# Performance work log

Measured on AMD Instinct MI355X. Metric: run time of the kernel, lower is better.

Reference implementation:

```python
import jax, jax.numpy as jnp
import numpy as np

DIM = 1024
HEADS = 8
HEAD_DIM = DIM // HEADS
FFN = 4096
B, N = 32, 1024
EPS = 1e-5


def layer_norm(x, g, b):
    mu = jnp.mean(x, axis=-1, keepdims=True)
    var = jnp.mean(jnp.square(x - mu), axis=-1, keepdims=True)
    return (x - mu) * jax.lax.rsqrt(var + EPS) * g + b


def setup_inputs() -> dict:
    key = jax.random.key(0)
    ks = jax.random.split(key, 10)
    s = 0.02
    return {
        "x": jax.random.normal(ks[0], (B, N, DIM), dtype=jnp.float32),
        "haltingscore": jnp.zeros((B, N), dtype=jnp.float32),
        "Wq": jax.random.normal(ks[1], (DIM, DIM), dtype=jnp.float32) * s,
        "Wkv": jax.random.normal(ks[2], (DIM, 2 * DIM), dtype=jnp.float32) * s,
        "Wp": jax.random.normal(ks[3], (DIM, DIM), dtype=jnp.float32) * s,
        "bp": jnp.zeros((DIM,), dtype=jnp.float32),
        "W1": jax.random.normal(ks[4], (DIM, FFN), dtype=jnp.float32) * s,
        "b1": jnp.zeros((FFN,), dtype=jnp.float32),
        "W2": jax.random.normal(ks[5], (FFN, DIM), dtype=jnp.float32) * s,
        "b2": jnp.zeros((DIM,), dtype=jnp.float32),
        "ln1_g": jnp.ones((DIM,), dtype=jnp.float32),
        "ln1_b": jnp.zeros((DIM,), dtype=jnp.float32),
        "ln2_g": jnp.ones((DIM,), dtype=jnp.float32),
        "ln2_b": jnp.zeros((DIM,), dtype=jnp.float32),
    }


def reference(x, haltingscore, Wq, Wkv, Wp, bp, W1, b1, W2, b2,
              ln1_g, ln1_b, ln2_g, ln2_b):
    b, n, c = x.shape
    scale = HEAD_DIM ** -0.5
    # ---- EfficientAttention (explicit QK^T softmax V) ----
    q = (x @ Wq).reshape(b, n, HEADS, HEAD_DIM).transpose(0, 2, 1, 3)  # bhnd
    kv = (x @ Wkv).reshape(b, n, 2, HEADS, HEAD_DIM).transpose(2, 0, 3, 1, 4)
    k, v = kv[0], kv[1]                                               # bhnd
    attn = jax.nn.softmax(jnp.einsum('bhnd,bhmd->bhnm', q, k) * scale, axis=-1)
    o = jnp.einsum('bhnm,bhmd->bhnd', attn, v)
    o = o.transpose(0, 2, 1, 3).reshape(b, n, c)
    o = o @ Wp + bp
    attn_mean = jnp.mean(attn, axis=1)                                # (B, N, N)
    # ---- residual + LN1 ----
    h = layer_norm(x + o, ln1_g, ln1_b)
    # ---- FFN + residual + LN2 ----
    ff = jax.nn.relu(h @ W1 + b1) @ W2 + b2
    out = layer_norm(h + ff, ln2_g, ln2_b)
    # ---- halting score update ----
    a = jax.nn.softmax(jnp.sum(attn_mean, axis=1), axis=-1)           # (B, N)
    halting = haltingscore + a
    return (out, halting, a)
```

## Files before the change

### kernel.cpp

```cpp
#include <hip/hip_runtime.h>
#include <hip/hip_bf16.h>
#include <stdint.h>

#define DIMC 1024
#define HEADS 8
#define HDIM 128
#define FFND 4096
#define BATCH 32
#define SEQ 1024
#define SROWS (BATCH*SEQ)
#define QSTR 3072

typedef unsigned short u16;
typedef short short4v __attribute__((ext_vector_type(4)));
typedef short short8 __attribute__((ext_vector_type(8)));
typedef float f32x4 __attribute__((ext_vector_type(4)));
typedef __bf16 bf16x8 __attribute__((ext_vector_type(8)));
typedef unsigned uintv2 __attribute__((ext_vector_type(2)));

__device__ __forceinline__ u16 f2bf(float f) {
    union { float f; uint32_t u; } x{f};
    uint32_t r = x.u + 0x7FFFu + ((x.u >> 16) & 1u);
    return (u16)(r >> 16);
}
__device__ __forceinline__ float bf2f(u16 h) {
    union { uint32_t u; float f; } x;
    x.u = ((uint32_t)h) << 16;
    return x.f;
}

__device__ __forceinline__ f32x4 mfma16(short8 a, short8 b, f32x4 c) {
    return __builtin_amdgcn_mfma_f32_16x16x32_bf16(
        __builtin_bit_cast(bf16x8, a), __builtin_bit_cast(bf16x8, b), c, 0, 0, 0);
}

__device__ __forceinline__ void gload_lds16(const u16* g, u16* lds) {
    __builtin_amdgcn_global_load_lds(
        (const __attribute__((address_space(1))) uint32_t*)g,
        (__attribute__((address_space(3))) uint32_t*)lds, 16, 0, 0);
}

#define DPP_RORADD(x, ctrl) do {                                               \
    int _t = __builtin_amdgcn_mov_dpp(__builtin_bit_cast(int, (x)), (ctrl),    \
                                      0xf, 0xf, true);                         \
    (x) += __builtin_bit_cast(float, _t); } while (0)

__device__ __forceinline__ short8 p2frag(f32x4 p0, f32x4 p1, int lane) {
    uint32_t a, b, c, d;
    asm("v_cvt_pk_bf16_f32 %0, %1, %2" : "=v"(a) : "v"(p0[0]), "v"(p0[1]));
    asm("v_cvt_pk_bf16_f32 %0, %1, %2" : "=v"(b) : "v"(p0[2]), "v"(p0[3]));
    asm("v_cvt_pk_bf16_f32 %0, %1, %2" : "=v"(c) : "v"(p1[0]), "v"(p1[1]));
    asm("v_cvt_pk_bf16_f32 %0, %1, %2" : "=v"(d) : "v"(p1[2]), "v"(p1[3]));
    uint32_t P, Q, R, S;
#if __has_builtin(__builtin_amdgcn_permlane32_swap)
    {
        uintv2 pq = __builtin_amdgcn_permlane32_swap(a, c, false, false);
        uintv2 rs = __builtin_amdgcn_permlane32_swap(b, d, false, false);
        P = pq[0]; Q = pq[1]; R = rs[0]; S = rs[1];
    }
#else
    {
        uint32_t ax = (uint32_t)__shfl_xor((int)a, 32);
        uint32_t bx = (uint32_t)__shfl_xor((int)b, 32);
        uint32_t cx = (uint32_t)__shfl_xor((int)c, 32);
        uint32_t dx = (uint32_t)__shfl_xor((int)d, 32);
        const bool up = (lane & 32) != 0;
        P = up ? cx : a; Q = up ? c : ax;
        R = up ? dx : b; S = up ? d : bx;
    }
#endif
    uint32_t w0, w1, w2, w3;
#if __has_builtin(__builtin_amdgcn_permlane16_swap)
    {
        uintv2 w02 = __builtin_amdgcn_permlane16_swap(P, Q, false, false);
        uintv2 w13 = __builtin_amdgcn_permlane16_swap(R, S, false, false);
        w0 = w02[0]; w2 = w02[1]; w1 = w13[0]; w3 = w13[1];
    }
#else
    {
        uint32_t Px = (uint32_t)__shfl_xor((int)P, 16);
        uint32_t Qx = (uint32_t)__shfl_xor((int)Q, 16);
        uint32_t Rx = (uint32_t)__shfl_xor((int)R, 16);
        uint32_t Sx = (uint32_t)__shfl_xor((int)S, 16);
        const bool odd = (lane & 16) != 0;
        w0 = odd ? Qx : P;  w1 = odd ? Sx : R;
        w2 = odd ? Q  : Px; w3 = odd ? S  : Rx;
    }
#endif
    union { uint32_t w[4]; short8 s; } u;
    u.w[0] = w0; u.w[1] = w1; u.w[2] = w2; u.w[3] = w3;
    return u.s;
}

__global__ __launch_bounds__(256) void k_cast(const float* __restrict__ in,
                                              u16* __restrict__ out, int n4) {
    int i = blockIdx.x * 256 + threadIdx.x;
    if (i < n4) {
        f32x4 v = ((const f32x4*)in)[i];
        uint32_t lo = f2bf(v[0]) | ((uint32_t)f2bf(v[1]) << 16);
        uint32_t hi = f2bf(v[2]) | ((uint32_t)f2bf(v[3]) << 16);
        ((uint2*)out)[i] = make_uint2(lo, hi);
    }
}

__global__ __launch_bounds__(256) void k_transpose_cast(const float* __restrict__ W,
                                                        u16* __restrict__ Wt,
                                                        int K, int N) {
    __shared__ u16 tile[32][33];
    int n0 = blockIdx.x * 32, k0 = blockIdx.y * 32;
    int tx = threadIdx.x, ty = threadIdx.y;
#pragma unroll
    for (int i = 0; i < 32; i += 8)
        tile[ty + i][tx] = f2bf(W[(size_t)(k0 + ty + i) * N + n0 + tx]);
    __syncthreads();
#pragma unroll
    for (int i = 0; i < 32; i += 8)
        Wt[(size_t)(n0 + ty + i) * K + k0 + tx] = tile[tx][ty + i];
}

template<bool OUT_BF16, bool RELU, bool BIAS, bool VSPLIT>
__global__ __launch_bounds__(512, 2) void k_gemm256(const u16* __restrict__ A,
                                                    const u16* __restrict__ Bt,
                                                    const float* __restrict__ bias,
                                                    void* __restrict__ C,
                                                    u16* __restrict__ Vt,
                                                    int M, int N, int K, int lda) {
    union Smem {
        struct { u16 A[4][8192]; u16 B[4][8192]; } k;
        u16 ob[64 * 264];
        float of[64 * 268];
        u16 vt[256 * 66];
    };
    __shared__ Smem smem;
    const int tid = threadIdx.x;
    const int lane = tid & 63, wv = tid >> 6;
    const int wm = wv >> 2, wn = wv & 3;
    const int l15 = lane & 15, lg = lane >> 4;
    const int gx = gridDim.x;
    const int nwg = gx * gridDim.y;
    const int id = blockIdx.y * gx + blockIdx.x;
    const int id2 = (id & 7) * (nwg >> 3) + (id >> 3);
    const int row0 = (id2 / gx) << 8, col0 = (id2 % gx) << 8;
    const int NT = K >> 5;

#define STAGE_A(tt) {                                                          \
    int _t = (tt);                                                             \
    _Pragma("unroll")                                                          \
    for (int i = 0; i < 2; ++i) {                                              \
        int blk = wv * 2 + i;                                                  \
        gload_lds16(A + (size_t)(row0 + blk * 16 + l15) * lda + _t * 32 + lg * 8,\
                    &smem.k.A[_t & 3][blk * 512]);                             \
    } }
#define STAGE_B(tt) {                                                          \
    int _t = (tt);                                                             \
    _Pragma("unroll")                                                          \
    for (int i = 0; i < 2; ++i) {                                              \
        int blk = wv * 2 + i;                                                  \
        gload_lds16(Bt + (size_t)(col0 + blk * 16 + l15) * K + _t * 32 + lg * 8,\
                    &smem.k.B[_t & 3][blk * 512]);                             \
    } }

    STAGE_A(0); STAGE_B(0);
    STAGE_A(1); STAGE_B(1);
    STAGE_A(2); STAGE_B(2);

    f32x4 acc[8][4] = {};
    for (int t = 0; t < NT; ++t) {
        const int slot = t & 3;
        if (t <= NT - 3)      asm volatile("s_waitcnt vmcnt(8)" ::: "memory");
        else if (t == NT - 2) asm volatile("s_waitcnt vmcnt(4)" ::: "memory");
        else                  asm volatile("s_waitcnt vmcnt(0)" ::: "memory");
        __builtin_amdgcn_s_barrier();
        __builtin_amdgcn_sched_barrier(0);

        const u16* Ab = &smem.k.A[slot][(wm * 8) * 512];
        const u16* Bb = &smem.k.B[slot][(wn * 4) * 512];

        if (t + 3 < NT) STAGE_A(t + 3);
        short8 bf[4], af[4];
#pragma unroll
        for (int n = 0; n < 4; ++n) bf[n] = *(const short8*)(Bb + n * 512 + lane * 8);
#pragma unroll
        for (int m = 0; m < 4; ++m) af[m] = *(const short8*)(Ab + m * 512 + lane * 8);
        __builtin_amdgcn_s_setprio(1);
#pragma unroll
        for (int m = 0; m < 4; ++m)
#pragma unroll
            for (int n = 0; n < 4; ++n)
                acc[m][n] = mfma16(af[m], bf[n], acc[m][n]);
        __builtin_amdgcn_s_setprio(0);

        if (t + 3 < NT) STAGE_B(t + 3);
#pragma unroll
        for (int m = 0; m < 4; ++m) af[m] = *(const short8*)(Ab + (4 + m) * 512 + lane * 8);
        __builtin_amdgcn_s_setprio(1);
#pragma unroll
        for (int m = 0; m < 4; ++m)
#pragma unroll
            for (int n = 0; n < 4; ++n)
                acc[4 + m][n] = mfma16(af[m], bf[n], acc[4 + m][n]);
        __builtin_amdgcn_s_setprio(0);
    }
#undef STAGE_A
#undef STAGE_B

    const bool vpath = VSPLIT && (col0 >= 2048);
    __syncthreads();
#pragma unroll
    for (int s = 0; s < 4; ++s) {
        if (s) __syncthreads();
        if (wm == (s >> 1)) {
            const int mb4 = (s & 1) * 4;
#pragma unroll
            for (int mm = 0; mm < 4; ++mm)
#pragma unroll
                for (int n = 0; n < 4; ++n) {
                    int c = wn * 64 + n * 16 + l15;
                    float bv = BIAS ? bias[col0 + c] : 0.f;
#pragma unroll
                    for (int j = 0; j < 4; ++j) {
                        int lr = mm * 16 + lg * 4 + j;
                        float v = acc[mb4 + mm][n][j] + bv;
                        if (RELU) v = fmaxf(v, 0.f);
                        if (vpath)         smem.vt[c * 66 + lr] = f2bf(v);
                        else if (OUT_BF16) smem.ob[lr * 264 + c] = f2bf(v);
                        else               smem.of[lr * 268 + c] = v;
                    }
                }
        }
        __syncthreads();
        const int gr0 = row0 + s * 64;
        if (vpath) {
            const int bb = gr0 >> 10;
            const int mb = gr0 & 1023;
#pragma unroll
            for (int it = 0; it < 4; ++it) {
                int idx = it * 512 + tid;
                int dc = idx >> 3, mseg = idx & 7;
                int hh = (col0 - 2048 + dc) >> 7;
                int dd = (col0 - 2048 + dc) & 127;
                *(short8*)(Vt + ((size_t)(bb * 8 + hh)) * (HDIM * SEQ)
                              + (size_t)dd * SEQ + mb + mseg * 8) =
                    *(const short8*)(&smem.vt[dc * 66 + mseg * 8]);
            }
        } else if (OUT_BF16) {
#pragma unroll
            for (int it = 0; it < 4; ++it) {
                int idx = it * 512 + tid;
                int r = idx >> 5, seg = idx & 31;
                *(short8*)((u16*)C + (size_t)(gr0 + r) * N + col0 + seg * 8) =
                    *(const short8*)(&smem.ob[r * 264 + seg * 8]);
            }
        } else {
#pragma unroll
            for (int it = 0; it < 8; ++it) {
                int idx = it * 512 + tid;
                int r = idx >> 6, seg = idx & 63;
                *(f32x4*)((float*)C + (size_t)(gr0 + r) * N + col0 + seg * 4) =
                    *(const f32x4*)(&smem.of[r * 268 + seg * 4]);
            }
        }
    }
}

__global__ __launch_bounds__(256, 3) void k_attn(const u16* __restrict__ QKV,
                                                 const u16* __restrict__ Vt,
                                                 u16* __restrict__ O,
                                                 float* __restrict__ csp) {
    union Sm {
        u16 K2[2][8192];
        struct { u16 Kl[2][4096]; u16 Vl[2][4096]; } pb;
    };
    __shared__ Sm sm;
    __shared__ float cs[1024];
    const int id = blockIdx.x;
    const int id2 = (id & 7) * 256 + (id >> 3);
    const int qt = id2 & 7, bh = id2 >> 3;
    const int b = bh >> 3, h = bh & 7;
    const int tid = threadIdx.x, lane = tid & 63, wv = tid >> 6;
    const int l15 = lane & 15, lg = lane >> 4;

    for (int i = tid; i < 1024; i += 256) cs[i] = 0.f;

    const int q0 = qt * 128 + wv * 32;
    const u16* qbaseA = QKV + (size_t)(b * SEQ + q0 + l15) * QSTR + h * HDIM + lg * 8;
    const u16* qbaseB = qbaseA + (size_t)16 * QSTR;
    short8 qfA[4], qfB[4];
#pragma unroll
    for (int kk = 0; kk < 4; ++kk) {
        qfA[kk] = *(const short8*)(qbaseA + kk * 32);
        qfB[kk] = *(const short8*)(qbaseB + kk * 32);
    }
    const float CEXP = 0.12751743f;
    const u16* kbase = QKV + (size_t)(b * SEQ) * QSTR + 1024 + h * HDIM;
    const u16* vtb = Vt + (size_t)bh * HDIM * SEQ;

#define STAGE_K2(tt) { _Pragma("unroll")                                        \
    for (int i = 0; i < 4; ++i) {                                               \
        gload_lds16(kbase + (size_t)((tt) * 64 + wv * 16 + l15) * QSTR          \
                    + i * 32 + lg * 8, &sm.K2[(tt) & 1][(wv * 4 + i) * 512]); } }
#define STAGE_K(tt) { _Pragma("unroll")                                         \
    for (int i = 0; i < 2; ++i) { int c = wv * 2 + i;                           \
        gload_lds16(kbase + (size_t)((tt) * 32 + (c >> 2) * 16 + l15) * QSTR    \
                    + (c & 3) * 32 + lg * 8, &sm.pb.Kl[(tt) & 1][c * 512]); } }
#define STAGE_V(tt) { _Pragma("unroll")                                         \
    for (int i = 0; i < 2; ++i) { int c = wv * 2 + i;                           \
        gload_lds16(vtb + (size_t)(c * 16 + l15) * SEQ + (tt) * 32 + lg * 8,    \
                    &sm.pb.Vl[(tt) & 1][c * 512]); } }

    STAGE_K2(0);
    asm volatile("s_waitcnt vmcnt(0)" ::: "memory");
    __builtin_amdgcn_s_barrier();
    f32x4 rsA4 = {0.f, 0.f, 0.f, 0.f}, rsB4 = {0.f, 0.f, 0.f, 0.f};
    for (int t = 0; t < 16; ++t) {
        if (t < 15) STAGE_K2(t + 1);
        const u16* Kp = &sm.K2[t & 1][0];
        __builtin_amdgcn_s_setprio(1);
#pragma unroll
        for (int j = 0; j < 4; j += 2) {
            f32x4 s0 = {0.f,0.f,0.f,0.f}, s1 = {0.f,0.f,0.f,0.f};
            f32x4 s2 = {0.f,0.f,0.f,0.f}, s3 = {0.f,0.f,0.f,0.f};
#pragma unroll
            for (int kk = 0; kk < 4; ++kk) {
                short8 k0 = *(const short8*)(Kp + (j * 4 + kk) * 512 + lane * 8);
                short8 k1 = *(const short8*)(Kp + ((j + 1) * 4 + kk) * 512 + lane * 8);
                s0 = mfma16(k0, qfA[kk], s0);
                s1 = mfma16(k0, qfB[kk], s1);
                s2 = mfma16(k1, qfA[kk], s2);
                s3 = mfma16(k1, qfB[kk], s3);
            }
#pragma unroll
            for (int r = 0; r < 4; ++r) {
                rsA4[r] += __builtin_amdgcn_exp2f(s0[r] * CEXP)
                         + __builtin_amdgcn_exp2f(s2[r] * CEXP);
                rsB4[r] += __builtin_amdgcn_exp2f(s1[r] * CEXP)
                         + __builtin_amdgcn_exp2f(s3[r] * CEXP);
            }
        }
        __builtin_amdgcn_s_setprio(0);
        asm volatile("s_waitcnt vmcnt(0)" ::: "memory");
        __builtin_amdgcn_s_barrier();
    }
    float rsA = (rsA4[0] + rsA4[1]) + (rsA4[2] + rsA4[3]);
    float rsB = (rsB4[0] + rsB4[1]) + (rsB4[2] + rsB4[3]);
    rsA += __shfl_xor(rsA, 16); rsA += __shfl_xor(rsA, 32);
    rsB += __shfl_xor(rsB, 16); rsB += __shfl_xor(rsB, 32);
    const float lgA = __builtin_amdgcn_logf(rsA);
    const float lgB = __builtin_amdgcn_logf(rsB);

    STAGE_K(0); STAGE_V(0);
    asm volatile("s_waitcnt vmcnt(0)" ::: "memory");
    __builtin_amdgcn_s_barrier();
    f32x4 odA[8] = {}, odB[8] = {};
    for (int t = 0; t < 32; ++t) {
        const int m0 = t * 32;
        if (t < 31) { STAGE_K(t + 1); STAGE_V(t + 1); }
        const u16* Kp = &sm.pb.Kl[t & 1][0];
        f32x4 sA0 = {0.f,0.f,0.f,0.f}, sA1 = {0.f,0.f,0.f,0.f};
        f32x4 sB0 = {0.f,0.f,0.f,0.f}, sB1 = {0.f,0.f,0.f,0.f};
        __builtin_amdgcn_s_setprio(1);
#pragma unroll
        for (int kk = 0; kk < 4; ++kk) {
            short8 k0 = *(const short8*)(Kp + kk * 512 + lane * 8);
            short8 k1 = *(const short8*)(Kp + (4 + kk) * 512 + lane * 8);
            sA0 = mfma16(k0, qfA[kk], sA0);
            sA1 = mfma16(k1, qfA[kk], sA1);
            sB0 = mfma16(k0, qfB[kk], sB0);
            sB1 = mfma16(k1, qfB[kk], sB1);
        }
        __builtin_amdgcn_s_setprio(0);
        f32x4 pA0, pA1, pB0, pB1;
#pragma unroll
        for (int r = 0; r < 4; ++r) {
            pA0[r] = __builtin_amdgcn_exp2f(__builtin_fmaf(sA0[r], CEXP, -lgA));
            pA1[r] = __builtin_amdgcn_exp2f(__builtin_fmaf(sA1[r], CEXP, -lgA));
            pB0[r] = __builtin_amdgcn_exp2f(__builtin_fmaf(sB0[r], CEXP, -lgB));
            pB1[r] = __builtin_amdgcn_exp2f(__builtin_fmaf(sB1[r], CEXP, -lgB));
        }
        float csv[8];
#pragma unroll
        for (int r = 0; r < 4; ++r) {
            csv[r]     = pA0[r] + pB0[r];
            csv[4 + r] = pA1[r] + pB1[r];
        }
#pragma unroll
        for (int j2 = 0; j2 < 8; ++j2) {
            DPP_RORADD(csv[j2], 0x128);
            DPP_RORADD(csv[j2], 0x124);
            DPP_RORADD(csv[j2], 0x122);
            DPP_RORADD(csv[j2], 0x121);
        }
        float cval = csv[0];
        cval = (l15 == 1) ? csv[1] : cval;
        cval = (l15 == 2) ? csv[2] : cval;
        cval = (l15 == 3) ? csv[3] : cval;
        cval = (l15 == 4) ? csv[4] : cval;
        cval = (l15 == 5) ? csv[5] : cval;
        cval = (l15 == 6) ? csv[6] : cval;
        cval = (l15 == 7) ? csv[7] : cval;
        if (l15 < 8) {
            int mw = (l15 < 4) ? (lg * 4 + l15) : (16 + lg * 4 + (l15 - 4));
            atomicAdd(&cs[m0 + mw], cval);
        }
        short8 paA = p2frag(pA0, pA1, lane);
        short8 paB = p2frag(pB0, pB1, lane);
        const u16* Vb_ = &sm.pb.Vl[t & 1][0];
        __builtin_amdgcn_s_setprio(1);
#pragma unroll
        for (int db = 0; db < 8; ++db) {
            short8 vf = *(const short8*)(Vb_ + db * 512 + lane * 8);
            odA[db] = mfma16(paA, vf, odA[db]);
            odB[db] = mfma16(paB, vf, odB[db]);
        }
        __builtin_amdgcn_s_setprio(0);
        asm volatile("s_waitcnt vmcnt(0)" ::: "memory");
        __builtin_amdgcn_s_barrier();
    }
#undef STAGE_K2
#undef STAGE_K
#undef STAGE_V
    __syncthreads();
    u16* obA = O + (size_t)(b * SEQ + q0 + lg * 4) * QSTR + h * HDIM + l15;
    u16* obB = obA + (size_t)16 * QSTR;
#pragma unroll
    for (int db = 0; db < 8; ++db)
#pragma unroll
        for (int r = 0; r < 4; ++r) {
            obA[(size_t)r * QSTR + db * 16] = f2bf(odA[db][r]);
            obB[(size_t)r * QSTR + db * 16] = f2bf(odB[db][r]);
        }
    for (int m = tid; m < 1024; m += 256)
        csp[((size_t)bh * 8 + qt) * 1024 + m] = cs[m];
}

__global__ __launch_bounds__(256) void k_ln1(u16* xio,
                                             const u16* __restrict__ pj,
                                             const float* __restrict__ g,
                                             const float* __restrict__ bt) {
    const int row = blockIdx.x;
    const int t = threadIdx.x, lane = t & 63, wv = t >> 6;
    short4v va = ((const short4v*)(xio + (size_t)row * DIMC))[t];
    short4v hv = ((const short4v*)(pj + (size_t)row * DIMC))[t];
    f32x4 s;
#pragma unroll
    for (int j = 0; j < 4; ++j) s[j] = bf2f((u16)va[j]) + bf2f((u16)hv[j]);
    float sum = s[0] + s[1] + s[2] + s[3];
    float sq = s[0]*s[0] + s[1]*s[1] + s[2]*s[2] + s[3]*s[3];
#pragma unroll
    for (int o = 1; o < 64; o <<= 1) { sum += __shfl_xor(sum, o); sq += __shfl_xor(sq, o); }
    __shared__ float red[8];
    if (lane == 0) { red[wv] = sum; red[4 + wv] = sq; }
    __syncthreads();
    sum = red[0] + red[1] + red[2] + red[3];
    sq  = red[4] + red[5] + red[6] + red[7];
    float mu = sum * (1.f / DIMC);
    float rstd = rsqrtf(sq * (1.f / DIMC) - mu * mu + 1e-5f);
    f32x4 gg = ((const f32x4*)g)[t];
    f32x4 bb = ((const f32x4*)bt)[t];
    uint32_t lo, hi;
    float o0 = (s[0] - mu) * rstd * gg[0] + bb[0];
    float o1 = (s[1] - mu) * rstd * gg[1] + bb[1];
    float o2 = (s[2] - mu) * rstd * gg[2] + bb[2];
    float o3 = (s[3] - mu) * rstd * gg[3] + bb[3];
    lo = f2bf(o0) | ((uint32_t)f2bf(o1) << 16);
    hi = f2bf(o2) | ((uint32_t)f2bf(o3) << 16);
    ((uint2*)(xio + (size_t)row * DIMC))[t] = make_uint2(lo, hi);
}

__global__ __launch_bounds__(256) void k_ln2(const u16* __restrict__ xa,
                                             const u16* __restrict__ f2,
                                             const float* __restrict__ g,
                                             const float* __restrict__ bt,
                                             float* __restrict__ of) {
    const int row = blockIdx.x;
    const int t = threadIdx.x, lane = t & 63, wv = t >> 6;
    short4v hv = ((const short4v*)(xa + (size_t)row * DIMC))[t];
    short4v fv = ((const short4v*)(f2 + (size_t)row * DIMC))[t];
    f32x4 s;
#pragma unroll
    for (int j = 0; j < 4; ++j) s[j] = bf2f((u16)hv[j]) + bf2f((u16)fv[j]);
    float sum = s[0] + s[1] + s[2] + s[3];
    float sq = s[0]*s[0] + s[1]*s[1] + s[2]*s[2] + s[3]*s[3];
#pragma unroll
    for (int o = 1; o < 64; o <<= 1) { sum += __shfl_xor(sum, o); sq += __shfl_xor(sq, o); }
    __shared__ float red[8];
    if (lane == 0) { red[wv] = sum; red[4 + wv] = sq; }
    __syncthreads();
    sum = red[0] + red[1] + red[2] + red[3];
    sq  = red[4] + red[5] + red[6] + red[7];
    float mu = sum * (1.f / DIMC);
    float rstd = rsqrtf(sq * (1.f / DIMC) - mu * mu + 1e-5f);
    f32x4 gg = ((const f32x4*)g)[t];
    f32x4 bb = ((const f32x4*)bt)[t];
    f32x4 o4;
#pragma unroll
    for (int j = 0; j < 4; ++j) o4[j] = (s[j] - mu) * rstd * gg[j] + bb[j];
    ((f32x4*)(of + (size_t)row * DIMC))[t] = o4;
}

__global__ __launch_bounds__(256) void k_halt(const float* __restrict__ csp,
                                              const float* __restrict__ hs,
                                              float* __restrict__ halt_out,
                                              float* __restrict__ a_out) {
    const int b = blockIdx.x, t = threadIdx.x, lane = t & 63, wv = t >> 6;
    const float* base = csp + (size_t)b * 65536;
    float acc[4] = {0.f, 0.f, 0.f, 0.f};
    for (int s2 = 0; s2 < 64; ++s2) {
#pragma unroll
        for (int j = 0; j < 4; ++j) acc[j] += base[(size_t)s2 * 1024 + j * 256 + t];
    }
    float mx = -1e30f;
#pragma unroll
    for (int j = 0; j < 4; ++j) { acc[j] *= 0.125f; mx = fmaxf(mx, acc[j]); }
#pragma unroll
    for (int o = 1; o < 64; o <<= 1) mx = fmaxf(mx, __shfl_xor(mx, o));
    __shared__ float red[8];
    if (lane == 0) red[wv] = mx;
    __syncthreads();
    mx = fmaxf(fmaxf(red[0], red[1]), fmaxf(red[2], red[3]));
    float e[4]; float sum = 0.f;
#pragma unroll
    for (int j = 0; j < 4; ++j) { e[j] = __expf(acc[j] - mx); sum += e[j]; }
#pragma unroll
    for (int o = 1; o < 64; o <<= 1) sum += __shfl_xor(sum, o);
    if (lane == 0) red[4 + wv] = sum;
    __syncthreads();
    sum = red[4] + red[5] + red[6] + red[7];
    float inv = 1.f / sum;
#pragma unroll
    for (int j = 0; j < 4; ++j) {
        int m = j * 256 + t;
        float a = e[j] * inv;
        a_out[b * SEQ + m] = a;
        halt_out[b * SEQ + m] = hs[b * SEQ + m] + a;
    }
}

extern "C" void kernel_launch(void* const* d_in, const int* in_sizes, int n_in,
                              void* d_out, int out_size, void* d_ws, size_t ws_size,
                              hipStream_t stream) {
    (void)in_sizes; (void)n_in; (void)out_size; (void)ws_size;
    const float* x   = (const float*)d_in[0];
    const float* hs  = (const float*)d_in[1];
    const float* Wq  = (const float*)d_in[2];
    const float* Wkv = (const float*)d_in[3];
    const float* Wp  = (const float*)d_in[4];
    const float* bp  = (const float*)d_in[5];
    const float* W1  = (const float*)d_in[6];
    const float* b1  = (const float*)d_in[7];
    const float* W2  = (const float*)d_in[8];
    const float* b2  = (const float*)d_in[9];
    const float* g1  = (const float*)d_in[10];
    const float* be1 = (const float*)d_in[11];
    const float* g2  = (const float*)d_in[12];
    const float* be2 = (const float*)d_in[13];

    float* out = (float*)d_out;
    float* halt_out = out + (size_t)SROWS * DIMC;
    float* a_out = halt_out + SROWS;

    char* w = (char*)d_ws;
    const size_t MB = 1024 * 1024;
    u16*  xb    = (u16*)(w);
    u16*  qkv   = (u16*)(w + 64 * MB);
    u16*  Vt    = (u16*)(w + 256 * MB);
    u16*  WqkvT = (u16*)(w + 320 * MB);
    u16*  WpT   = (u16*)(w + 326 * MB);
    u16*  W1T   = (u16*)(w + 328 * MB);
    u16*  W2T   = (u16*)(w + 336 * MB);
    float* csp  = (float*)(w + 344 * MB);
    u16*  o_b   = qkv + 2048;
    u16*  projb = (u16*)(w + 256 * MB);
    u16*  hb    = xb;
    u16*  ff1   = (u16*)(w + 64 * MB);
    u16*  ff2b  = (u16*)(w + 192 * MB);

    dim3 tb(32, 8);
    k_cast<<<SROWS * DIMC / 4 / 256, 256, 0, stream>>>(x, xb, SROWS * DIMC / 4);
    k_transpose_cast<<<dim3(DIMC / 32, DIMC / 32), tb, 0, stream>>>(Wq, WqkvT, DIMC, DIMC);
    k_transpose_cast<<<dim3(2 * DIMC / 32, DIMC / 32), tb, 0, stream>>>(
        Wkv, WqkvT + (size_t)DIMC * DIMC, DIMC, 2 * DIMC);
    k_transpose_cast<<<dim3(DIMC / 32, DIMC / 32), tb, 0, stream>>>(Wp, WpT, DIMC, DIMC);
    k_transpose_cast<<<dim3(FFND / 32, DIMC / 32), tb, 0, stream>>>(W1, W1T, DIMC, FFND);
    k_transpose_cast<<<dim3(DIMC / 32, FFND / 32), tb, 0, stream>>>(W2, W2T, FFND, DIMC);
    k_gemm256<true, false, false, true><<<dim3(QSTR / 256, SROWS / 256), 512, 0, stream>>>(
        xb, WqkvT, nullptr, qkv, Vt, SROWS, QSTR, DIMC, DIMC);
    k_attn<<<2048, 256, 0, stream>>>(qkv, Vt, o_b, csp);
    k_gemm256<true, false, true, false><<<dim3(DIMC / 256, SROWS / 256), 512, 0, stream>>>(
        o_b, WpT, bp, projb, nullptr, SROWS, DIMC, DIMC, QSTR);
    k_ln1<<<SROWS, 256, 0, stream>>>(xb, projb, g1, be1);
    for (int c = 0; c < 2; ++c) {
        const size_t ro = (size_t)c * 16384;
        k_gemm256<true, true, true, false><<<dim3(FFND / 256, 16384 / 256), 512, 0, stream>>>(
            hb + ro * DIMC, W1T, b1, ff1, nullptr, 16384, FFND, DIMC, DIMC);
        k_gemm256<true, false, true, false><<<dim3(DIMC / 256, 16384 / 256), 512, 0, stream>>>(
            ff1, W2T, b2, ff2b, nullptr, 16384, DIMC, FFND, FFND);
        k_ln2<<<16384, 256, 0, stream>>>(hb + ro * DIMC, ff2b, g2, be2, out + ro * DIMC);
    }
    k_halt<<<BATCH, 256, 0, stream>>>(csp, hs, halt_out, a_out);
}
```

Measured before the change: 1.433 ms.

## Add two-slot ring GEMM variant, merge FFN chunks, fuse W2 output into LN2

```diff
diff --git a/kernel.cpp b/kernel.cpp
--- a/kernel.cpp
+++ b/kernel.cpp
@@ -118,15 +118,16 @@
         Wt[(size_t)(n0 + ty + i) * K + k0 + tx] = tile[tx][ty + i];
 }
 
-template<bool OUT_BF16, bool RELU, bool BIAS, bool VSPLIT>
-__global__ __launch_bounds__(512, 2) void k_gemm256(const u16* __restrict__ A,
+template<bool OUT_BF16, bool RELU, bool BIAS, bool VSPLIT, int RING>
+__global__ __launch_bounds__(512, RING == 2 ? 4 : 2) void k_gemm256(
+                                                    const u16* __restrict__ A,
                                                     const u16* __restrict__ Bt,
                                                     const float* __restrict__ bias,
                                                     void* __restrict__ C,
                                                     u16* __restrict__ Vt,
                                                     int M, int N, int K, int lda) {
     union Smem {
-        struct { u16 A[4][8192]; u16 B[4][8192]; } k;
+        struct { u16 A[RING][8192]; u16 B[RING][8192]; } k;
         u16 ob[64 * 264];
         float of[64 * 268];
         u16 vt[256 * 66];
@@ -149,7 +150,7 @@
     for (int i = 0; i < 2; ++i) {                                              \
         int blk = wv * 2 + i;                                                  \
         gload_lds16(A + (size_t)(row0 + blk * 16 + l15) * lda + _t * 32 + lg * 8,\
-                    &smem.k.A[_t & 3][blk * 512]);                             \
+                    &smem.k.A[_t & (RING - 1)][blk * 512]);                    \
     } }
 #define STAGE_B(tt) {                                                          \
     int _t = (tt);                                                             \
@@ -157,26 +158,38 @@
     for (int i = 0; i < 2; ++i) {                                              \
         int blk = wv * 2 + i;                                                  \
         gload_lds16(Bt + (size_t)(col0 + blk * 16 + l15) * K + _t * 32 + lg * 8,\
-                    &smem.k.B[_t & 3][blk * 512]);                             \
+                    &smem.k.B[_t & (RING - 1)][blk * 512]);                    \
     } }
 
-    STAGE_A(0); STAGE_B(0);
-    STAGE_A(1); STAGE_B(1);
-    STAGE_A(2); STAGE_B(2);
+    if constexpr (RING == 4) {
+        STAGE_A(0); STAGE_B(0);
+        STAGE_A(1); STAGE_B(1);
+        STAGE_A(2); STAGE_B(2);
+    } else {
+        STAGE_A(0); STAGE_B(0);
+        asm volatile("s_waitcnt vmcnt(0)" ::: "memory");
+        __builtin_amdgcn_s_barrier();
+    }
 
     f32x4 acc[8][4] = {};
     for (int t = 0; t < NT; ++t) {
-        const int slot = t & 3;
-        if (t <= NT - 3)      asm volatile("s_waitcnt vmcnt(8)" ::: "memory");
-        else if (t == NT - 2) asm volatile("s_waitcnt vmcnt(4)" ::: "memory");
-        else                  asm volatile("s_waitcnt vmcnt(0)" ::: "memory");
-        __builtin_amdgcn_s_barrier();
-        __builtin_amdgcn_sched_barrier(0);
+        const int slot = t & (RING - 1);
+        if constexpr (RING == 4) {
+            if (t <= NT - 3)      asm volatile("s_waitcnt vmcnt(8)" ::: "memory");
+            else if (t == NT - 2) asm volatile("s_waitcnt vmcnt(4)" ::: "memory");
+            else                  asm volatile("s_waitcnt vmcnt(0)" ::: "memory");
+            __builtin_amdgcn_s_barrier();
+            __builtin_amdgcn_sched_barrier(0);
+        }
 
         const u16* Ab = &smem.k.A[slot][(wm * 8) * 512];
         const u16* Bb = &smem.k.B[slot][(wn * 4) * 512];
 
-        if (t + 3 < NT) STAGE_A(t + 3);
+        if constexpr (RING == 4) {
+            if (t + 3 < NT) STAGE_A(t + 3);
+        } else {
+            if (t + 1 < NT) { STAGE_A(t + 1); STAGE_B(t + 1); }
+        }
         short8 bf[4], af[4];
 #pragma unroll
         for (int n = 0; n < 4; ++n) bf[n] = *(const short8*)(Bb + n * 512 + lane * 8);
@@ -190,7 +203,9 @@
                 acc[m][n] = mfma16(af[m], bf[n], acc[m][n]);
         __builtin_amdgcn_s_setprio(0);
 
-        if (t + 3 < NT) STAGE_B(t + 3);
+        if constexpr (RING == 4) {
+            if (t + 3 < NT) STAGE_B(t + 3);
+        }
 #pragma unroll
         for (int m = 0; m < 4; ++m) af[m] = *(const short8*)(Ab + (4 + m) * 512 + lane * 8);
         __builtin_amdgcn_s_setprio(1);
@@ -200,6 +215,13 @@
             for (int n = 0; n < 4; ++n)
                 acc[4 + m][n] = mfma16(af[m], bf[n], acc[4 + m][n]);
         __builtin_amdgcn_s_setprio(0);
+
+        if constexpr (RING == 2) {
+            if (t + 1 < NT) {
+                asm volatile("s_waitcnt vmcnt(0)" ::: "memory");
+                __builtin_amdgcn_s_barrier();
+            }
+        }
     }
 #undef STAGE_A
 #undef STAGE_B
@@ -263,7 +285,7 @@
     }
 }
 
-__global__ __launch_bounds__(256, 3) void k_attn(const u16* __restrict__ QKV,
+__global__ __launch_bounds__(256, 4) void k_attn(const u16* __restrict__ QKV,
                                                  const u16* __restrict__ Vt,
                                                  u16* __restrict__ O,
                                                  float* __restrict__ csp) {
@@ -468,17 +490,16 @@
 }
 
 __global__ __launch_bounds__(256) void k_ln2(const u16* __restrict__ xa,
-                                             const u16* __restrict__ f2,
                                              const float* __restrict__ g,
                                              const float* __restrict__ bt,
                                              float* __restrict__ of) {
     const int row = blockIdx.x;
     const int t = threadIdx.x, lane = t & 63, wv = t >> 6;
     short4v hv = ((const short4v*)(xa + (size_t)row * DIMC))[t];
-    short4v fv = ((const short4v*)(f2 + (size_t)row * DIMC))[t];
+    f32x4 fv = ((const f32x4*)(of + (size_t)row * DIMC))[t];
     f32x4 s;
 #pragma unroll
-    for (int j = 0; j < 4; ++j) s[j] = bf2f((u16)hv[j]) + bf2f((u16)fv[j]);
+    for (int j = 0; j < 4; ++j) s[j] = bf2f((u16)hv[j]) + fv[j];
     float sum = s[0] + s[1] + s[2] + s[3];
     float sq = s[0]*s[0] + s[1]*s[1] + s[2]*s[2] + s[3]*s[3];
 #pragma unroll
@@ -573,7 +594,6 @@
     u16*  projb = (u16*)(w + 256 * MB);
     u16*  hb    = xb;
     u16*  ff1   = (u16*)(w + 64 * MB);
-    u16*  ff2b  = (u16*)(w + 192 * MB);
 
     dim3 tb(32, 8);
     k_cast<<<SROWS * DIMC / 4 / 256, 256, 0, stream>>>(x, xb, SROWS * DIMC / 4);
@@ -583,19 +603,16 @@
     k_transpose_cast<<<dim3(DIMC / 32, DIMC / 32), tb, 0, stream>>>(Wp, WpT, DIMC, DIMC);
     k_transpose_cast<<<dim3(FFND / 32, DIMC / 32), tb, 0, stream>>>(W1, W1T, DIMC, FFND);
     k_transpose_cast<<<dim3(DIMC / 32, FFND / 32), tb, 0, stream>>>(W2, W2T, FFND, DIMC);
-    k_gemm256<true, false, false, true><<<dim3(QSTR / 256, SROWS / 256), 512, 0, stream>>>(
+    k_gemm256<true, false, false, true, 4><<<dim3(QSTR / 256, SROWS / 256), 512, 0, stream>>>(
         xb, WqkvT, nullptr, qkv, Vt, SROWS, QSTR, DIMC, DIMC);
     k_attn<<<2048, 256, 0, stream>>>(qkv, Vt, o_b, csp);
-    k_gemm256<true, false, true, false><<<dim3(DIMC / 256, SROWS / 256), 512, 0, stream>>>(
+    k_gemm256<true, false, true, false, 4><<<dim3(DIMC / 256, SROWS / 256), 512, 0, stream>>>(
         o_b, WpT, bp, projb, nullptr, SROWS, DIMC, DIMC, QSTR);
     k_ln1<<<SROWS, 256, 0, stream>>>(xb, projb, g1, be1);
-    for (int c = 0; c < 2; ++c) {
-        const size_t ro = (size_t)c * 16384;
-        k_gemm256<true, true, true, false><<<dim3(FFND / 256, 16384 / 256), 512, 0, stream>>>(
-            hb + ro * DIMC, W1T, b1, ff1, nullptr, 16384, FFND, DIMC, DIMC);
-        k_gemm256<true, false, true, false><<<dim3(DIMC / 256, 16384 / 256), 512, 0, stream>>>(
-            ff1, W2T, b2, ff2b, nullptr, 16384, DIMC, FFND, FFND);
-        k_ln2<<<16384, 256, 0, stream>>>(hb + ro * DIMC, ff2b, g2, be2, out + ro * DIMC);
-    }
+    k_gemm256<true, true, true, false, 4><<<dim3(FFND / 256, SROWS / 256), 512, 0, stream>>>(
+        hb, W1T, b1, ff1, nullptr, SROWS, FFND, DIMC, DIMC);
+    k_gemm256<false, false, true, false, 2><<<dim3(DIMC / 256, SROWS / 256), 512, 0, stream>>>(
+        ff1, W2T, b2, out, nullptr, SROWS, DIMC, FFND, FFND);
+    k_ln2<<<SROWS, 256, 0, stream>>>(hb, g2, be2, out);
     k_halt<<<BATCH, 256, 0, stream>>>(csp, hs, halt_out, a_out);
 }
```

After: 3.758 ms. +162.2%, slower.
